# Optimization experiments

Measured on AMD Instinct MI355X. Metric: run time of the kernel, lower is better.

Reference implementation:

```python
import jax, jax.numpy as jnp
import numpy as np

B, S, D, H, DK, DV = 4, 2048, 1024, 16, 64, 64
LN_EPS = 1e-5

def setup_inputs() -> dict:
    key = jax.random.key(0)
    ks = jax.random.split(key, 5)
    s = 0.02  # init scale for weights
    return {
        "tokens": jax.random.normal(ks[0], (B, S, D), jnp.float32),
        "Wq": jax.random.normal(ks[1], (H, D, DK), jnp.float32) * s,
        "Wk": jax.random.normal(ks[2], (H, D, DK), jnp.float32) * s,
        "Wv": jax.random.normal(ks[3], (H, D, DV), jnp.float32) * s,
        "Wo": jax.random.normal(ks[4], (H * DV, D), jnp.float32) * s,
        "gamma": jnp.ones((D,), jnp.float32),
        "beta": jnp.zeros((D,), jnp.float32),
    }

def reference(tokens, Wq, Wk, Wv, Wo, gamma, beta):
    # tokens: [B,S,D]; Wq/Wk: [H,D,DK]; Wv: [H,D,DV]; Wo: [H*DV, D]
    d_k = Wq.shape[-1]
    q = jnp.einsum('bsd,hdk->bhsk', tokens, Wq)
    k = jnp.einsum('bsd,hdk->bhsk', tokens, Wk)
    v = jnp.einsum('bsd,hdv->bhsv', tokens, Wv)
    # Faithful quirk of the original: attention() returns (Q K^T / sqrt(d_k)).transpose,
    # so attn[b,h,j,i] = q_i . k_j / sqrt(d_k) and softmax runs over the QUERY index i.
    attn = jnp.einsum('bhik,bhjk->bhji', q, k) / jnp.sqrt(jnp.float32(d_k))
    attn = jax.nn.softmax(attn, axis=-1)
    heads = jnp.einsum('bhji,bhiv->bhjv', attn, v)          # [B,H,S,DV]
    b, s = tokens.shape[0], tokens.shape[1]
    multi = jnp.transpose(heads, (0, 2, 1, 3)).reshape(b, s, -1)  # concat heads
    out = multi @ Wo + tokens                                # out-proj + residual
    mu = jnp.mean(out, axis=-1, keepdims=True)
    var = jnp.var(out, axis=-1, keepdims=True)
    out = (out - mu) / jnp.sqrt(var + LN_EPS) * gamma + beta  # LayerNorm
    return out
```

## Files before the change

### kernel.cpp

```cpp
#include <hip/hip_runtime.h>
#include <hip/hip_bf16.h>
#include <stdint.h>

typedef __attribute__((ext_vector_type(4))) float f32x4;
typedef __attribute__((ext_vector_type(16))) float f32x16;
typedef __attribute__((ext_vector_type(8))) short bf16x8;
typedef __attribute__((ext_vector_type(4))) unsigned short u16x4;
typedef unsigned short u16;
typedef uint32_t u32;

#define B_ 4
#define S_ 2048
#define D_ 1024
#define H_ 16
#define DK_ 64
#define BS_ (B_*S_)
#define NQKV_ (3*H_*DK_)
#define NT_ (S_/64)

#define QSCALE 0.18033688011112042f

__device__ __forceinline__ u16 f2bf(float x) {
  union { float f; uint32_t u; } c; c.f = x;
  uint32_t r = (c.u + 0x7FFFu + ((c.u >> 16) & 1u)) >> 16;
  return (u16)r;
}

__device__ __forceinline__ float bf2f(u16 x) {
  union { uint32_t u; float f; } c; c.u = ((uint32_t)x) << 16;
  return c.f;
}

__device__ __forceinline__ float exp2_fast(float x) {
  float r; asm("v_exp_f32 %0, %1" : "=v"(r) : "v"(x)); return r;
}

__device__ __forceinline__ void gl_lds16(const u16* g, u16* l) {
  __builtin_amdgcn_global_load_lds(
      (const __attribute__((address_space(1))) u32*)g,
      (__attribute__((address_space(3))) u32*)l, 16, 0, 0);
}

__global__ __launch_bounds__(256) void conv_f32_to_bf16(
    const float* __restrict__ src, u16* __restrict__ dst, int n) {
  int i = (blockIdx.x * 256 + threadIdx.x) * 4;
  if (i >= n) return;
  const float* p = src + i;
  u16x4 o = { f2bf(p[0]), f2bf(p[1]), f2bf(p[2]), f2bf(p[3]) };
  *(u16x4*)(dst + i) = o;
}

__global__ __launch_bounds__(256) void prep_weights(
    const float* __restrict__ Wq, const float* __restrict__ Wk,
    const float* __restrict__ Wv, const float* __restrict__ Wo,
    u16* __restrict__ wcatT, u16* __restrict__ woT) {
  __shared__ float Tl[64][65];
  const int y = blockIdx.y;
  if (y < 48) {
    const int w = y >> 4, hh = y & 15;
    const int d0 = blockIdx.x * 64;
    const float scale = (w == 0) ? QSCALE : 1.0f;
    const float* src = (w == 0 ? Wq : (w == 1 ? Wk : Wv)) + (long)hh * D_ * DK_;
    {
      int r = threadIdx.x >> 2, c = (threadIdx.x & 3) * 16;
      const float* g = src + (long)(d0 + r) * DK_ + c;
#pragma unroll
      for (int j = 0; j < 16; ++j) Tl[r][c + j] = g[j];
    }
    __syncthreads();
    {
      int dk = threadIdx.x >> 2, c = (threadIdx.x & 3) * 16;
      __attribute__((aligned(16))) u16 tmp[16];
#pragma unroll
      for (int j = 0; j < 16; ++j) tmp[j] = f2bf(Tl[c + j][dk] * scale);
      u16* o = wcatT + ((long)y * 64 + dk) * D_ + d0 + c;
      *(bf16x8*)o = *(const bf16x8*)&tmp[0];
      *(bf16x8*)(o + 8) = *(const bf16x8*)&tmp[8];
    }
  } else {
    const int r0 = (y - 48) * 64, c0 = blockIdx.x * 64;
    {
      int r = threadIdx.x >> 2, c = (threadIdx.x & 3) * 16;
      const float* g = Wo + (long)(r0 + r) * D_ + c0 + c;
#pragma unroll
      for (int j = 0; j < 16; ++j) Tl[r][c + j] = g[j];
    }
    __syncthreads();
    {
      int rr = threadIdx.x >> 2, c = (threadIdx.x & 3) * 16;
      __attribute__((aligned(16))) u16 tmp[16];
#pragma unroll
      for (int j = 0; j < 16; ++j) tmp[j] = f2bf(Tl[c + j][rr]);
      u16* o = woT + (long)(c0 + rr) * D_ + r0 + c;
      *(bf16x8*)o = *(const bf16x8*)&tmp[0];
      *(bf16x8*)(o + 8) = *(const bf16x8*)&tmp[8];
    }
  }
}

template<bool OUT_BF16, bool VSPLIT>
__global__ __launch_bounds__(256) void gemm_bf16(
    const u16* __restrict__ A, const u16* __restrict__ BT,
    void* __restrict__ Cout, const u16* __restrict__ resid,
    u16* __restrict__ vtout, int M, int N, int K) {
  __shared__ __attribute__((aligned(16))) u16 Al[3][128][32];
  __shared__ __attribute__((aligned(16))) u16 Bl[3][128][32];
  const int tid = threadIdx.x;
  const int wid = tid >> 6;
  const int lane = tid & 63;
  const int wm = (wid >> 1) * 64;
  const int wn = (wid & 1) * 64;
  const int row0 = blockIdx.x * 128;
  const int col0 = blockIdx.y * 128;
  const int fr = lane & 15;
  const int g = lane >> 4;

  const int srow = lane >> 2;
  const int sch = lane & 3;
  const int r0a = 32 * wid + srow;
  f32x4 acc[4][4] = {};

#define GSTAGE(bufi, kk)                                                       \
  {                                                                            \
    _Pragma("unroll")                                                          \
    for (int s = 0; s < 2; ++s) {                                              \
      int r = r0a + 16 * s;                                                    \
      int gc = (sch ^ ((r >> 1) & 3)) * 8;                                     \
      gl_lds16(A + (long)(row0 + r) * K + (kk) + gc, &Al[bufi][32 * wid + 16 * s][0]); \
      gl_lds16(BT + (long)(col0 + r) * K + (kk) + gc, &Bl[bufi][32 * wid + 16 * s][0]); \
    }                                                                          \
  }

  const int nt = K >> 5;
  GSTAGE(0, 0);

  for (int t = 0; t < nt; ++t) {
    const int cur = t % 3;
    if (t + 1 < nt) {
      GSTAGE((t + 1) % 3, (t + 1) << 5);
      asm volatile("s_waitcnt vmcnt(4)" ::: "memory");
    } else {
      asm volatile("s_waitcnt vmcnt(0)" ::: "memory");
    }
    __builtin_amdgcn_s_barrier();
    asm volatile("" ::: "memory");

    bf16x8 af[4], bfr[4];
#pragma unroll
    for (int mf = 0; mf < 4; ++mf) {
      int row = wm + mf * 16 + fr;
      af[mf] = *(const bf16x8*)&Al[cur][row][(g ^ ((row >> 1) & 3)) * 8];
    }
#pragma unroll
    for (int nf = 0; nf < 4; ++nf) {
      int row = wn + nf * 16 + fr;
      bfr[nf] = *(const bf16x8*)&Bl[cur][row][(g ^ ((row >> 1) & 3)) * 8];
    }
    __builtin_amdgcn_s_setprio(1);
#pragma unroll
    for (int mf = 0; mf < 4; ++mf)
#pragma unroll
      for (int nf = 0; nf < 4; ++nf)
        acc[mf][nf] = __builtin_amdgcn_mfma_f32_16x16x32_bf16(
            af[mf], bfr[nf], acc[mf][nf], 0, 0, 0);
    __builtin_amdgcn_s_setprio(0);
  }
#undef GSTAGE

  const int r0 = (lane >> 4) * 4;
  if constexpr (VSPLIT) {
    if (col0 >= 2048) {
#pragma unroll
      for (int mf = 0; mf < 4; ++mf)
#pragma unroll
        for (int nf = 0; nf < 4; ++nf) {
          int colv = col0 + wn + nf * 16 + fr - 2048;
          long row = row0 + wm + mf * 16 + r0;
          int b2 = (int)(row >> 11);
          int i = (int)(row & 2047);
          u16x4 o = { f2bf(acc[mf][nf][0]), f2bf(acc[mf][nf][1]),
                      f2bf(acc[mf][nf][2]), f2bf(acc[mf][nf][3]) };
          *(u16x4*)(vtout + ((long)(b2 * 16 + (colv >> 6)) * 64 + (colv & 63)) * S_ + i) = o;
        }
      return;
    }
  }
#pragma unroll
  for (int mf = 0; mf < 4; ++mf)
#pragma unroll
    for (int nf = 0; nf < 4; ++nf)
#pragma unroll
      for (int r = 0; r < 4; ++r) {
        long row = row0 + wm + mf * 16 + r0 + r;
        long col = col0 + wn + nf * 16 + fr;
        if constexpr (OUT_BF16) {
          ((u16*)Cout)[row * N + col] = f2bf(acc[mf][nf][r]);
        } else {
          float v = acc[mf][nf][r] + bf2f(resid[row * N + col]);
          ((float*)Cout)[row * N + col] = v;
        }
      }
}

__global__ __launch_bounds__(512, 4) void attn_kernel(
    const u16* __restrict__ qkv, const u16* __restrict__ vt,
    u16* __restrict__ multi) {
  __shared__ __attribute__((aligned(16))) u16 smem[3][2][64][64];
  const int tid = threadIdx.x;
  const int wid = tid >> 6;
  const int lane = tid & 63;
  const int jl = lane & 31;
  const int h = lane >> 5;

  const int bid = blockIdx.x;
  const int bh = bid & 63;
  const int jt = bid >> 6;
  const int b = bh >> 4, hh = bh & 15;
  const long rowb = (long)b * S_;
  const long rj0 = rowb + (long)jt * 256 + wid * 32;
  const int cbQ = hh * 64, cbK = (H_ + hh) * 64;

#define XF(r) (((r) ^ ((r) >> 3)) & 7)

  bf16x8 kf[4];
  const u16* kbase = qkv + (rj0 + jl) * NQKV_ + cbK + 8 * h;
#pragma unroll
  for (int ks = 0; ks < 4; ++ks) kf[ks] = *(const bf16x8*)(kbase + 16 * ks);

  const int strow = 8 * wid + (lane >> 3);
  const int stoff = ((lane & 7) ^ XF(strow)) * 8;
  const u16* qsrc = qkv + (rowb + strow) * NQKV_ + cbQ + stoff;
  const u16* vsrc = vt + ((long)bh * 64 + strow) * S_ + stoff;

  f32x16 accT0 = {}, accT1 = {};
  float l0 = 0.f, l1 = 0.f, l2 = 0.f, l3 = 0.f;

  gl_lds16(qsrc, &smem[0][0][8 * wid][0]);
  gl_lds16(vsrc, &smem[0][1][8 * wid][0]);
  qsrc += (long)64 * NQKV_; vsrc += 64;

  for (int it = 0; it < NT_; ++it) {
    const int cur = it % 3;
    if (it + 1 < NT_) {
      const int nx = (it + 1) % 3;
      gl_lds16(qsrc, &smem[nx][0][8 * wid][0]);
      gl_lds16(vsrc, &smem[nx][1][8 * wid][0]);
      qsrc += (long)64 * NQKV_; vsrc += 64;
      asm volatile("s_waitcnt vmcnt(2)" ::: "memory");
    } else {
      asm volatile("s_waitcnt vmcnt(0)" ::: "memory");
    }
    __builtin_amdgcn_s_barrier();
    asm volatile("" ::: "memory");

#pragma unroll
    for (int mb = 0; mb < 2; ++mb) {
      const int qrow = 32 * mb + jl;
      f32x16 st = {};
      __builtin_amdgcn_s_setprio(1);
#pragma unroll
      for (int ks = 0; ks < 4; ++ks) {
        bf16x8 qf = *(const bf16x8*)&smem[cur][0][qrow][((2 * ks + h) ^ XF(qrow)) * 8];
        st = __builtin_amdgcn_mfma_f32_32x32x16_bf16(qf, kf[ks], st, 0, 0, 0);
      }
      __builtin_amdgcn_s_setprio(0);

      uint32_t q32[8];
#pragma unroll
      for (int rp = 0; rp < 8; ++rp) {
        float p0 = exp2_fast(st[2 * rp]);
        float p1 = exp2_fast(st[2 * rp + 1]);
        if (rp & 1) { l2 += p0; l3 += p1; } else { l0 += p0; l1 += p1; }
        __hip_bfloat162 bb = __float22bfloat162_rn(make_float2(p0, p1));
        uint32_t w; __builtin_memcpy(&w, &bb, 4);
        q32[rp] = w;
      }

      __builtin_amdgcn_s_setprio(1);
#pragma unroll
      for (int t2 = 0; t2 < 2; ++t2) {
        const int ks = 2 * mb + t2;
        uint32_t a0 = q32[4 * t2 + 0], b0 = q32[4 * t2 + 1];
        uint32_t a1 = q32[4 * t2 + 2], b1 = q32[4 * t2 + 3];
        asm("v_permlane32_swap_b32 %0, %1" : "+v"(a0), "+v"(a1));
        asm("v_permlane32_swap_b32 %0, %1" : "+v"(b0), "+v"(b1));
        union { bf16x8 v; uint32_t u[4]; } pa;
        pa.u[0] = a0; pa.u[1] = b0; pa.u[2] = a1; pa.u[3] = b1;
        bf16x8 vf0 = *(const bf16x8*)&smem[cur][1][jl][((2 * ks + h) ^ XF(jl)) * 8];
        bf16x8 vf1 = *(const bf16x8*)&smem[cur][1][32 + jl][((2 * ks + h) ^ XF(32 + jl)) * 8];
        accT0 = __builtin_amdgcn_mfma_f32_32x32x16_bf16(vf0, pa.v, accT0, 0, 0, 0);
        accT1 = __builtin_amdgcn_mfma_f32_32x32x16_bf16(vf1, pa.v, accT1, 0, 0, 0);
      }
      __builtin_amdgcn_s_setprio(0);
    }
  }
#undef XF

  __syncthreads();
  u16 (*Wl)[32][72] = (u16 (*)[32][72])&smem[0][0][0][0];
  float lsum = (l0 + l2) + (l1 + l3);
  lsum += __shfl_xor(lsum, 32);
  float inv = 1.f / lsum;
#pragma unroll
  for (int r = 0; r < 16; ++r) {
    int d = (r & 3) + 8 * (r >> 2) + 4 * h;
    Wl[wid][jl][d] = f2bf(accT0[r] * inv);
    Wl[wid][jl][32 + d] = f2bf(accT1[r] * inv);
  }
  int j2 = lane >> 1, dh = (lane & 1) * 32;
#pragma unroll
  for (int c = 0; c < 4; ++c) {
    bf16x8 vrow = *(const bf16x8*)&Wl[wid][j2][dh + 8 * c];
    *(bf16x8*)(multi + (rj0 + j2) * (H_ * DK_) + hh * 64 + dh + 8 * c) = vrow;
  }
}

__global__ __launch_bounds__(256) void ln_kernel(
    float* __restrict__ out, const float* __restrict__ gamma,
    const float* __restrict__ beta) {
  const int tid = threadIdx.x;
  const int wid = tid >> 6;
  const int lane = tid & 63;
  float* p = out + (long)blockIdx.x * D_;
  const float* pv = p + tid * 4;
  float x0 = pv[0], x1 = pv[1], x2 = pv[2], x3 = pv[3];
  float s = x0 + x1 + x2 + x3;
  float q = x0 * x0 + x1 * x1 + x2 * x2 + x3 * x3;
#pragma unroll
  for (int off = 32; off > 0; off >>= 1) {
    s += __shfl_down(s, off);
    q += __shfl_down(q, off);
  }
  __shared__ float sh[8];
  if (lane == 0) { sh[wid] = s; sh[4 + wid] = q; }
  __syncthreads();
  s = sh[0] + sh[1] + sh[2] + sh[3];
  q = sh[4] + sh[5] + sh[6] + sh[7];
  float mean = s * (1.0f / D_);
  float var = q * (1.0f / D_) - mean * mean;
  float rstd = rsqrtf(var + 1e-5f);
  const float* g = gamma + tid * 4;
  const float* be = beta + tid * 4;
  float* po = p + tid * 4;
  po[0] = (x0 - mean) * rstd * g[0] + be[0];
  po[1] = (x1 - mean) * rstd * g[1] + be[1];
  po[2] = (x2 - mean) * rstd * g[2] + be[2];
  po[3] = (x3 - mean) * rstd * g[3] + be[3];
}

extern "C" void kernel_launch(void* const* d_in, const int* in_sizes, int n_in,
                              void* d_out, int out_size, void* d_ws, size_t ws_size,
                              hipStream_t stream) {
  const float* tokens = (const float*)d_in[0];
  const float* Wq = (const float*)d_in[1];
  const float* Wk = (const float*)d_in[2];
  const float* Wv = (const float*)d_in[3];
  const float* Wo = (const float*)d_in[4];
  const float* gamma = (const float*)d_in[5];
  const float* beta = (const float*)d_in[6];
  float* out = (float*)d_out;

  char* ws = (char*)d_ws;
  u16* tok_bf = (u16*)(ws);
  u16* wcatT  = (u16*)(ws + 16777216);
  u16* woT    = (u16*)(ws + 23068672);
  u16* qkv    = (u16*)(ws + 25165824);
  u16* multi  = (u16*)(ws + 75497472);
  u16* vt     = (u16*)(ws + 92274688);

  conv_f32_to_bf16<<<8192, 256, 0, stream>>>(tokens, tok_bf, BS_ * D_);
  prep_weights<<<dim3(16, 64), 256, 0, stream>>>(Wq, Wk, Wv, Wo, wcatT, woT);

  gemm_bf16<true, true><<<dim3(BS_ / 128, NQKV_ / 128), 256, 0, stream>>>(
      tok_bf, wcatT, qkv, nullptr, vt, BS_, NQKV_, D_);

  attn_kernel<<<512, 512, 0, stream>>>(qkv, vt, multi);

  gemm_bf16<false, false><<<dim3(BS_ / 128, D_ / 128), 256, 0, stream>>>(
      multi, woT, out, tok_bf, nullptr, BS_, D_, D_);

  ln_kernel<<<BS_, 256, 0, stream>>>(out, gamma, beta);
}
```

Measured before the change: 195.0 us.

## Merge prep kernels, widen GEMM tiles to 128x256, swizzle blocks, bf16 pre-LN output

Folds the token conversion and the weight transpose into a single prep launch. The GEMMs now use 512-thread blocks with 128x256 tiles and an XCD-aware block remapping, which improves B-tile reuse and L2 locality. The out-projection writes bf16 back into the token buffer in place, so the layernorm reads bf16 instead of fp32 and less traffic moves between stages. In exchange, the pre-layernorm values are rounded to bf16, and the in-place write to the residual buffer relies on each element being read before it is overwritten by the same thread.

```diff
diff --git a/kernel.cpp b/kernel.cpp
--- a/kernel.cpp
+++ b/kernel.cpp
@@ -41,24 +41,25 @@
       (__attribute__((address_space(3))) u32*)l, 16, 0, 0);
 }
 
-__global__ __launch_bounds__(256) void conv_f32_to_bf16(
-    const float* __restrict__ src, u16* __restrict__ dst, int n) {
-  int i = (blockIdx.x * 256 + threadIdx.x) * 4;
-  if (i >= n) return;
-  const float* p = src + i;
-  u16x4 o = { f2bf(p[0]), f2bf(p[1]), f2bf(p[2]), f2bf(p[3]) };
-  *(u16x4*)(dst + i) = o;
-}
-
-__global__ __launch_bounds__(256) void prep_weights(
-    const float* __restrict__ Wq, const float* __restrict__ Wk,
-    const float* __restrict__ Wv, const float* __restrict__ Wo,
+__global__ __launch_bounds__(256) void prep_all(
+    const float* __restrict__ tokens, const float* __restrict__ Wq,
+    const float* __restrict__ Wk, const float* __restrict__ Wv,
+    const float* __restrict__ Wo, u16* __restrict__ tok_bf,
     u16* __restrict__ wcatT, u16* __restrict__ woT) {
+  const int bid = blockIdx.x;
+  if (bid < 8192) {
+    int i = (bid * 256 + threadIdx.x) * 4;
+    const float* p = tokens + i;
+    u16x4 o = { f2bf(p[0]), f2bf(p[1]), f2bf(p[2]), f2bf(p[3]) };
+    *(u16x4*)(tok_bf + i) = o;
+    return;
+  }
   __shared__ float Tl[64][65];
-  const int y = blockIdx.y;
-  if (y < 48) {
+  const int t = bid - 8192;
+  if (t < 768) {
+    const int y = t >> 4, xx = t & 15;
     const int w = y >> 4, hh = y & 15;
-    const int d0 = blockIdx.x * 64;
+    const int d0 = xx * 64;
     const float scale = (w == 0) ? QSCALE : 1.0f;
     const float* src = (w == 0 ? Wq : (w == 1 ? Wk : Wv)) + (long)hh * D_ * DK_;
     {
@@ -78,7 +79,8 @@
       *(bf16x8*)(o + 8) = *(const bf16x8*)&tmp[8];
     }
   } else {
-    const int r0 = (y - 48) * 64, c0 = blockIdx.x * 64;
+    const int t2 = t - 768;
+    const int r0 = (t2 >> 4) * 64, c0 = (t2 & 15) * 64;
     {
       int r = threadIdx.x >> 2, c = (threadIdx.x & 3) * 16;
       const float* g = Wo + (long)(r0 + r) * D_ + c0 + c;
@@ -98,47 +100,49 @@
   }
 }
 
-template<bool OUT_BF16, bool VSPLIT>
-__global__ __launch_bounds__(256) void gemm_bf16(
+template<bool RESID, bool VSPLIT>
+__global__ __launch_bounds__(512, 2) void gemm_bf16(
     const u16* __restrict__ A, const u16* __restrict__ BT,
-    void* __restrict__ Cout, const u16* __restrict__ resid,
-    u16* __restrict__ vtout, int M, int N, int K) {
+    u16* Cout, const u16* resid,
+    u16* __restrict__ vtout, int M, int N, int K, int gx) {
   __shared__ __attribute__((aligned(16))) u16 Al[3][128][32];
-  __shared__ __attribute__((aligned(16))) u16 Bl[3][128][32];
+  __shared__ __attribute__((aligned(16))) u16 Bl[3][256][32];
   const int tid = threadIdx.x;
   const int wid = tid >> 6;
   const int lane = tid & 63;
-  const int wm = (wid >> 1) * 64;
-  const int wn = (wid & 1) * 64;
-  const int row0 = blockIdx.x * 128;
-  const int col0 = blockIdx.y * 128;
+  const int wm = (wid >> 2) * 64;
+  const int wn = (wid & 3) * 64;
+  const int per = (int)gridDim.x >> 3;
+  const int g = ((int)blockIdx.x & 7) * per + ((int)blockIdx.x >> 3);
+  const int row0 = (g % gx) * 128;
+  const int col0 = (g / gx) * 256;
   const int fr = lane & 15;
-  const int g = lane >> 4;
-
+  const int gch = lane >> 4;
   const int srow = lane >> 2;
   const int sch = lane & 3;
-  const int r0a = 32 * wid + srow;
+
+  const int rA = 16 * wid + srow;
+  const int rB0 = 32 * wid + srow;
+  const int rB1 = rB0 + 16;
+  const u16* aptr = A + (long)(row0 + rA) * K + (sch ^ ((rA >> 1) & 3)) * 8;
+  const u16* bptr0 = BT + (long)(col0 + rB0) * K + (sch ^ ((rB0 >> 1) & 3)) * 8;
+  const u16* bptr1 = BT + (long)(col0 + rB1) * K + (sch ^ ((rB1 >> 1) & 3)) * 8;
+
   f32x4 acc[4][4] = {};
-
-#define GSTAGE(bufi, kk)                                                       \
-  {                                                                            \
-    _Pragma("unroll")                                                          \
-    for (int s = 0; s < 2; ++s) {                                              \
-      int r = r0a + 16 * s;                                                    \
-      int gc = (sch ^ ((r >> 1) & 3)) * 8;                                     \
-      gl_lds16(A + (long)(row0 + r) * K + (kk) + gc, &Al[bufi][32 * wid + 16 * s][0]); \
-      gl_lds16(BT + (long)(col0 + r) * K + (kk) + gc, &Bl[bufi][32 * wid + 16 * s][0]); \
-    }                                                                          \
-  }
-
   const int nt = K >> 5;
-  GSTAGE(0, 0);
-
+
+#define GSTAGE(bufi)                                                           \
+  { gl_lds16(aptr, &Al[bufi][16 * wid][0]);                                    \
+    gl_lds16(bptr0, &Bl[bufi][32 * wid][0]);                                   \
+    gl_lds16(bptr1, &Bl[bufi][32 * wid + 16][0]);                              \
+    aptr += 32; bptr0 += 32; bptr1 += 32; }
+
+  GSTAGE(0);
   for (int t = 0; t < nt; ++t) {
     const int cur = t % 3;
     if (t + 1 < nt) {
-      GSTAGE((t + 1) % 3, (t + 1) << 5);
-      asm volatile("s_waitcnt vmcnt(4)" ::: "memory");
+      GSTAGE((t + 1) % 3);
+      asm volatile("s_waitcnt vmcnt(3)" ::: "memory");
     } else {
       asm volatile("s_waitcnt vmcnt(0)" ::: "memory");
     }
@@ -149,12 +153,12 @@
 #pragma unroll
     for (int mf = 0; mf < 4; ++mf) {
       int row = wm + mf * 16 + fr;
-      af[mf] = *(const bf16x8*)&Al[cur][row][(g ^ ((row >> 1) & 3)) * 8];
+      af[mf] = *(const bf16x8*)&Al[cur][row][(gch ^ ((row >> 1) & 3)) * 8];
     }
 #pragma unroll
     for (int nf = 0; nf < 4; ++nf) {
       int row = wn + nf * 16 + fr;
-      bfr[nf] = *(const bf16x8*)&Bl[cur][row][(g ^ ((row >> 1) & 3)) * 8];
+      bfr[nf] = *(const bf16x8*)&Bl[cur][row][(gch ^ ((row >> 1) & 3)) * 8];
     }
     __builtin_amdgcn_s_setprio(1);
 #pragma unroll
@@ -193,11 +197,11 @@
       for (int r = 0; r < 4; ++r) {
         long row = row0 + wm + mf * 16 + r0 + r;
         long col = col0 + wn + nf * 16 + fr;
-        if constexpr (OUT_BF16) {
-          ((u16*)Cout)[row * N + col] = f2bf(acc[mf][nf][r]);
+        if constexpr (RESID) {
+          float v = acc[mf][nf][r] + bf2f(resid[row * N + col]);
+          Cout[row * N + col] = f2bf(v);
         } else {
-          float v = acc[mf][nf][r] + bf2f(resid[row * N + col]);
-          ((float*)Cout)[row * N + col] = v;
+          Cout[row * N + col] = f2bf(acc[mf][nf][r]);
         }
       }
 }
@@ -316,14 +320,14 @@
 }
 
 __global__ __launch_bounds__(256) void ln_kernel(
-    float* __restrict__ out, const float* __restrict__ gamma,
-    const float* __restrict__ beta) {
+    const u16* __restrict__ outb, float* __restrict__ out,
+    const float* __restrict__ gamma, const float* __restrict__ beta) {
   const int tid = threadIdx.x;
   const int wid = tid >> 6;
   const int lane = tid & 63;
-  float* p = out + (long)blockIdx.x * D_;
-  const float* pv = p + tid * 4;
-  float x0 = pv[0], x1 = pv[1], x2 = pv[2], x3 = pv[3];
+  const u16* pb = outb + (long)blockIdx.x * D_ + tid * 4;
+  u16x4 v = *(const u16x4*)pb;
+  float x0 = bf2f(v.x), x1 = bf2f(v.y), x2 = bf2f(v.z), x3 = bf2f(v.w);
   float s = x0 + x1 + x2 + x3;
   float q = x0 * x0 + x1 * x1 + x2 * x2 + x3 * x3;
 #pragma unroll
@@ -341,7 +345,7 @@
   float rstd = rsqrtf(var + 1e-5f);
   const float* g = gamma + tid * 4;
   const float* be = beta + tid * 4;
-  float* po = p + tid * 4;
+  float* po = out + (long)blockIdx.x * D_ + tid * 4;
   po[0] = (x0 - mean) * rstd * g[0] + be[0];
   po[1] = (x1 - mean) * rstd * g[1] + be[1];
   po[2] = (x2 - mean) * rstd * g[2] + be[2];
@@ -368,16 +372,15 @@
   u16* multi  = (u16*)(ws + 75497472);
   u16* vt     = (u16*)(ws + 92274688);
 
-  conv_f32_to_bf16<<<8192, 256, 0, stream>>>(tokens, tok_bf, BS_ * D_);
-  prep_weights<<<dim3(16, 64), 256, 0, stream>>>(Wq, Wk, Wv, Wo, wcatT, woT);
-
-  gemm_bf16<true, true><<<dim3(BS_ / 128, NQKV_ / 128), 256, 0, stream>>>(
-      tok_bf, wcatT, qkv, nullptr, vt, BS_, NQKV_, D_);
+  prep_all<<<9216, 256, 0, stream>>>(tokens, Wq, Wk, Wv, Wo, tok_bf, wcatT, woT);
+
+  gemm_bf16<false, true><<<768, 512, 0, stream>>>(
+      tok_bf, wcatT, qkv, nullptr, vt, BS_, NQKV_, D_, 64);
 
   attn_kernel<<<512, 512, 0, stream>>>(qkv, vt, multi);
 
-  gemm_bf16<false, false><<<dim3(BS_ / 128, D_ / 128), 256, 0, stream>>>(
-      multi, woT, out, tok_bf, nullptr, BS_, D_, D_);
-
-  ln_kernel<<<BS_, 256, 0, stream>>>(out, gamma, beta);
-}
+  gemm_bf16<true, false><<<256, 512, 0, stream>>>(
+      multi, woT, tok_bf, tok_bf, nullptr, BS_, D_, D_, 64);
+
+  ln_kernel<<<BS_, 256, 0, stream>>>(tok_bf, out, gamma, beta);
+}
```

Result: slower. 204.6 us (+4.9%).
